# Kernel tuning notes

Hardware: AMD Instinct MI355X
Metric: run time of the kernel (lower is better)

The kernel has to match this reference:

```python
import jax, jax.numpy as jnp
import numpy as np
import math

NUM_HEADS = 16
SEQ_LEN = 2048
K_OFFSET = 37
P = 2


def get_slopes(n):
    def pow2(m):
        start = 2 ** (-2 ** (-(math.log2(m) - 3)))
        return [start * start ** i for i in range(m)]
    if math.log2(n).is_integer():
        return pow2(n)
    c = 2 ** math.floor(math.log2(n))
    return pow2(c) + get_slopes(2 * c)[0::2][: n - c]


def setup_inputs() -> dict:
    key = jax.random.key(0)
    k1, k2, k3 = jax.random.split(key, 3)
    x = jax.random.normal(k1, (2, 2048, 1024), jnp.float32)  # only dtype is used
    # delta ~ Gamma(concentration=2, rate=1), shape (P, d) with d=1
    delta = jax.random.gamma(k2, 2.0, (P, 1)).astype(jnp.float32)
    # u ~ Uniform(0, delta)
    u = jax.random.uniform(k3, (P, 1), jnp.float32) * delta
    return {"x": x, "delta": delta, "u": u, "seq_len": SEQ_LEN, "k": K_OFFSET}


def reference(x, delta, u, seq_len, k):
    dtype = x.dtype
    N = seq_len
    # positions t = arange(k, seq_len + k), shape (N, 1) == rbf input X
    t = jnp.arange(k, seq_len + k, dtype=dtype).reshape(-1, 1)

    def one_binning(delta_p, u_p):
        # ceil-binning; since t is strictly increasing, bin ids are nondecreasing,
        # so torch.unique's inverse_indices == cumulative rank of bin changes.
        idx = jnp.ceil((t - u_p) / delta_p).astype(jnp.int32)       # (N, 1)
        change = jnp.any(idx[1:] != idx[:-1], axis=-1).astype(jnp.int32)  # (N-1,)
        inv = jnp.concatenate([jnp.zeros((1,), jnp.int32), jnp.cumsum(change)])  # (N,)
        # one-hot over unique bins, padded to N columns (extra columns are zero)
        return (inv[:, None] == jnp.arange(N, dtype=jnp.int32)[None, :]).astype(dtype)

    Zp = jax.vmap(one_binning)(delta, u)                 # (P, N, N)
    Pn = Zp.shape[0]
    Z = jnp.transpose(Zp, (1, 0, 2)).reshape(N, Pn * N)  # hstack over P
    Z = Z / jnp.sqrt(jnp.asarray(Pn, dtype))

    slopes = jnp.asarray(get_slopes(NUM_HEADS), dtype)
    sqrt_slopes = jnp.sqrt(jnp.exp(slopes)).reshape(NUM_HEADS, 1, 1)
    alibi = (sqrt_slopes * Z[None, :, :])[None]          # (1, H, N, P*N)
    return jnp.transpose(alibi, (2, 0, 1, 3))            # (N, 1, H, P*N)
```

## Files before the change

kernel.cpp:

```cpp
#include <hip/hip_runtime.h>
#include <hip/hip_bf16.h>


#define N_SEQ 2048
#define H_NUM 16
#define P_NUM 2

__global__ void binning_kernel(const float* __restrict__ delta,
                               const float* __restrict__ u,
                               const int* __restrict__ kptr,
                               int* __restrict__ inv) {
    const int p = blockIdx.x;
    const int t = threadIdx.x;
    const float dp = delta[p];
    const float up = u[p];
    const int kk = kptr[0];

    __shared__ int s[2][N_SEQ];

    for (int j = t; j < N_SEQ; j += 1024) {
        int idx = (int)ceilf(((float)(kk + j) - up) / dp);
        int flag = 0;
        if (j > 0) {
            int idxm = (int)ceilf(((float)(kk + j - 1) - up) / dp);
            flag = (idx != idxm) ? 1 : 0;
        }
        s[0][j] = flag;
    }
    __syncthreads();

    int src = 0;
    for (int off = 1; off < N_SEQ; off <<= 1) {
        int dst = src ^ 1;
        for (int j = t; j < N_SEQ; j += 1024) {
            int v = s[src][j];
            if (j >= off) v += s[src][j - off];
            s[dst][j] = v;
        }
        __syncthreads();
        src = dst;
    }

    for (int j = t; j < N_SEQ; j += 1024)
        inv[p * N_SEQ + j] = s[src][j];
}

__global__ __launch_bounds__(256) void scatter_kernel(const int* __restrict__ inv,
                                                      float* __restrict__ out) {
    const int e = blockIdx.x * 256 + threadIdx.x;
    const int n = e >> 5;
    const int h = (e >> 1) & 15;
    const int p = e & 1;

    const float slope = exp2f(-0.5f * (float)(h + 1));
    const float val = sqrtf(expf(slope)) * 0.70710678118f;

    const int col = inv[p * N_SEQ + n];
    const size_t addr = (size_t)((n << 4) + h) * 4096u + (size_t)(p << 11) + (size_t)col;
    out[addr] = val;
}

extern "C" void kernel_launch(void* const* d_in, const int* in_sizes, int n_in,
                              void* d_out, int out_size, void* d_ws, size_t ws_size,
                              hipStream_t stream) {
    const float* delta = (const float*)d_in[1];
    const float* u     = (const float*)d_in[2];
    const int*   kptr  = (const int*)d_in[4];
    int* inv = (int*)d_ws;

    binning_kernel<<<P_NUM, 1024, 0, stream>>>(delta, u, kptr, inv);

    hipMemsetAsync(d_out, 0, (size_t)out_size * sizeof(float), stream);

    scatter_kernel<<<(N_SEQ * H_NUM * P_NUM) / 256, 256, 0, stream>>>(inv, (float*)d_out);
}
```

Before: 103.7 us.

## Fuse binning scan into scatter kernel with per-block redundant prefix counts

Removes the separate single-block binning/scan kernel and its workspace round trip. Each scatter block now recomputes the bin-change count up to its first row, using a block-wide reduction plus a small per-block prefix over its 8 rows. This saves one launch and the serial scan, at the cost of redundant ceil/div work that grows with block index.

Result: faster. 100.5 us (-3.1%).

```diff
diff --git a/kernel.cpp b/kernel.cpp
--- a/kernel.cpp
+++ b/kernel.cpp
@@ -6,58 +6,63 @@
 #define H_NUM 16
 #define P_NUM 2
 
-__global__ void binning_kernel(const float* __restrict__ delta,
-                               const float* __restrict__ u,
-                               const int* __restrict__ kptr,
-                               int* __restrict__ inv) {
-    const int p = blockIdx.x;
-    const int t = threadIdx.x;
-    const float dp = delta[p];
-    const float up = u[p];
-    const int kk = kptr[0];
+__device__ __forceinline__ int bin_idx(int kk, int m, float up, float dp) {
+    return (int)ceilf(((float)(kk + m) - up) / dp);
+}
 
-    __shared__ int s[2][N_SEQ];
+__global__ __launch_bounds__(256) void scan_scatter_kernel(
+        const float* __restrict__ delta, const float* __restrict__ u,
+        const int* __restrict__ kptr, float* __restrict__ out) {
+    const int blk = blockIdx.x;
+    const int tid = threadIdx.x;
+    const int n0  = blk << 3;
+    const int kk  = kptr[0];
 
-    for (int j = t; j < N_SEQ; j += 1024) {
-        int idx = (int)ceilf(((float)(kk + j) - up) / dp);
-        int flag = 0;
-        if (j > 0) {
-            int idxm = (int)ceilf(((float)(kk + j - 1) - up) / dp);
-            flag = (idx != idxm) ? 1 : 0;
+    __shared__ int s_cnt[P_NUM];
+    __shared__ int s_wpre[P_NUM][8];
+
+    if (tid < P_NUM) s_cnt[tid] = 0;
+    if (tid < P_NUM) {
+        const int p = tid;
+        const float dp = delta[p], up = u[p];
+        int acc = 0;
+        s_wpre[p][0] = 0;
+        int prev = bin_idx(kk, n0, up, dp);
+        for (int d = 1; d < 8; ++d) {
+            int cur = bin_idx(kk, n0 + d, up, dp);
+            acc += (cur != prev) ? 1 : 0;
+            prev = cur;
+            s_wpre[p][d] = acc;
         }
-        s[0][j] = flag;
     }
     __syncthreads();
 
-    int src = 0;
-    for (int off = 1; off < N_SEQ; off <<= 1) {
-        int dst = src ^ 1;
-        for (int j = t; j < N_SEQ; j += 1024) {
-            int v = s[src][j];
-            if (j >= off) v += s[src][j - off];
-            s[dst][j] = v;
+    {
+        const int p = tid >> 7;
+        const float dp = delta[p], up = u[p];
+        int local = 0;
+        for (int m = 1 + (tid & 127); m <= n0; m += 128) {
+            int a = bin_idx(kk, m,     up, dp);
+            int b = bin_idx(kk, m - 1, up, dp);
+            local += (a != b) ? 1 : 0;
         }
-        __syncthreads();
-        src = dst;
+        #pragma unroll
+        for (int off = 32; off > 0; off >>= 1)
+            local += __shfl_down(local, off, 64);
+        if ((tid & 63) == 0) atomicAdd(&s_cnt[p], local);
     }
+    __syncthreads();
 
-    for (int j = t; j < N_SEQ; j += 1024)
-        inv[p * N_SEQ + j] = s[src][j];
-}
-
-__global__ __launch_bounds__(256) void scatter_kernel(const int* __restrict__ inv,
-                                                      float* __restrict__ out) {
-    const int e = blockIdx.x * 256 + threadIdx.x;
-    const int n = e >> 5;
-    const int h = (e >> 1) & 15;
-    const int p = e & 1;
+    const int dn = tid >> 5;
+    const int h  = (tid >> 1) & 15;
+    const int p  = tid & 1;
+    const int n  = n0 + dn;
+    const int col = s_cnt[p] + s_wpre[p][dn];
 
     const float slope = exp2f(-0.5f * (float)(h + 1));
     const float val = sqrtf(expf(slope)) * 0.70710678118f;
 
-    const int col = inv[p * N_SEQ + n];
-    const size_t addr = (size_t)((n << 4) + h) * 4096u + (size_t)(p << 11) + (size_t)col;
-    out[addr] = val;
+    out[(size_t)((n << 4) + h) * 4096u + (size_t)(p << 11) + (size_t)col] = val;
 }
 
 extern "C" void kernel_launch(void* const* d_in, const int* in_sizes, int n_in,
@@ -66,11 +71,8 @@
     const float* delta = (const float*)d_in[1];
     const float* u     = (const float*)d_in[2];
     const int*   kptr  = (const int*)d_in[4];
-    int* inv = (int*)d_ws;
-
-    binning_kernel<<<P_NUM, 1024, 0, stream>>>(delta, u, kptr, inv);
 
     hipMemsetAsync(d_out, 0, (size_t)out_size * sizeof(float), stream);
 
-    scatter_kernel<<<(N_SEQ * H_NUM * P_NUM) / 256, 256, 0, stream>>>(inv, (float*)d_out);
+    scan_scatter_kernel<<<256, 256, 0, stream>>>(delta, u, kptr, (float*)d_out);
 }
```
